# Kernel tuning notes

Measured on AMD Instinct MI355X. Metric: run time of the kernel, lower is better.

Reference implementation:

```python
import jax, jax.numpy as jnp
import numpy as np

H = 256
B, S = 8, 2048
WIN = 16


def setup_inputs() -> dict:
    key = jax.random.key(0)
    k1, k2, k3, k4, k5 = jax.random.split(key, 5)
    bound = 1.0 / np.sqrt(H)  # torch nn.RNN init range
    x = jax.random.normal(k1, (B, S, H), dtype=jnp.float32)
    W_ih = jax.random.uniform(k2, (H, H), jnp.float32, -bound, bound)
    W_hh = jax.random.uniform(k3, (H, H), jnp.float32, -bound, bound)
    b_ih = jax.random.uniform(k4, (H,), jnp.float32, -bound, bound)
    b_hh = jax.random.uniform(k5, (H,), jnp.float32, -bound, bound)
    return {"x": x, "W_ih": W_ih, "W_hh": W_hh, "b_ih": b_ih, "b_hh": b_hh, "window": WIN}


def reference(x, W_ih, W_hh, b_ih, b_hh, window):
    # Original: get_K builds [B, S, window, H] overlapping windows (left-padded
    # with window-1 zeros), runs an RNN over each length-`window` sequence with
    # h0 = 0, and keeps the last hidden state -> [B, S, H].
    # Equivalent streaming form: at step k of the window, every position t
    # consumes xpad[:, t + k]; so slice a shifted view of the padded input and
    # update all B*S hidden states at once (never materializing the windows).
    b, s, h = x.shape
    xpad = jnp.pad(x, ((0, 0), (window - 1, 0), (0, 0)))  # [B, S+W-1, H]

    def step(hid, k):
        xk = jax.lax.dynamic_slice(xpad, (0, k, 0), (b, s, h))  # [B, S, H]
        hid = jnp.tanh(xk @ W_ih.T + b_ih + hid @ W_hh.T + b_hh)
        return hid, None

    h0 = jnp.zeros((b, s, h), dtype=x.dtype)
    h_last, _ = jax.lax.scan(step, h0, jnp.arange(window))
    return h_last  # [B, S, H]
```

## Files before the change

### kernel.cpp

```cpp
#include <hip/hip_runtime.h>

#define HDIM 256
#define SEQ 2048
#define TPOS 32

typedef _Float16 half8_t __attribute__((ext_vector_type(8)));
typedef float floatx16 __attribute__((ext_vector_type(16)));

#define U_PITCH 1024
#define H_PITCH 512
#define U_ROWS 47
#define H0_OFF (U_ROWS * U_PITCH)
#define H1_OFF (H0_OFF + 32 * H_PITCH)
#define LDS_BYTES (H0_OFF + 2 * 32 * H_PITCH)

static __device__ __forceinline__ float exp2f_fast(float x) {
  float r; asm("v_exp_f32 %0, %1" : "=v"(r) : "v"(x)); return r;
}
static __device__ __forceinline__ float rcpf_fast(float x) {
  float r; asm("v_rcp_f32 %0, %1" : "=v"(r) : "v"(x)); return r;
}
static __device__ __forceinline__ float tanhf_fast(float x) {
  float e = exp2f_fast(x * 2.8853900817779268f);
  return 1.0f - 2.0f * rcpf_fast(e + 1.0f);
}
static __device__ __forceinline__ unsigned pkh(float a, float b) {
  return __builtin_bit_cast(unsigned, __builtin_amdgcn_cvt_pkrtz(a, b));
}

__global__ __launch_bounds__(256, 2) void winrnn_kernel(
    const float* __restrict__ x, const float* __restrict__ W_ih,
    const float* __restrict__ W_hh, const float* __restrict__ b_ih,
    const float* __restrict__ b_hh, float* __restrict__ out) {
  extern __shared__ char smem[];
  const int tid = threadIdx.x;
  const int w = tid >> 6;
  const int lane = tid & 63;
  const int l31 = lane & 31;
  const int hi = lane >> 5;

  const int wg = blockIdx.x;
  const int batch = wg >> 6;
  const int t0 = (wg & 63) * TPOS;
  const float* xb = x + (size_t)batch * SEQ * HDIM;

  const int jbase = w * 64;
  const int p_loc = l31;
  const int hswz = l31 << 4;

  {
    char* xl = smem + H0_OFF;
#pragma unroll
    for (int it = 0; it < 16; ++it) {
      int idx = tid + it * 256;
      int row = idx >> 6;
      int c4 = idx & 63;
      int xi = t0 - 15 + row;
      float4 v = make_float4(0.f, 0.f, 0.f, 0.f);
      if (row < U_ROWS && xi >= 0)
        v = *reinterpret_cast<const float4*>(xb + (size_t)xi * HDIM + c4 * 4);
      uint2 u;
      u.x = pkh(v.x, v.y);
      u.y = pkh(v.z, v.w);
      *reinterpret_cast<uint2*>(xl + row * H_PITCH + ((c4 * 8) ^ ((row & 31) << 4))) = u;
    }
  }

  half8_t Wf[2][16];
#pragma unroll
  for (int jt = 0; jt < 2; ++jt)
#pragma unroll
    for (int kt = 0; kt < 16; ++kt) {
      const float* wp = W_ih + (size_t)(jbase + jt * 32 + l31) * HDIM + kt * 16 + hi * 8;
      float4 a = *reinterpret_cast<const float4*>(wp);
      float4 b = *reinterpret_cast<const float4*>(wp + 4);
      uint4 uu;
      uu.x = pkh(a.x, a.y); uu.y = pkh(a.z, a.w);
      uu.z = pkh(b.x, b.y); uu.w = pkh(b.z, b.w);
      Wf[jt][kt] = __builtin_bit_cast(half8_t, uu);
    }

  float4 biasf[2][4];
#pragma unroll
  for (int jt = 0; jt < 2; ++jt)
#pragma unroll
    for (int g = 0; g < 4; ++g) {
      int j0 = jbase + jt * 32 + g * 8 + hi * 4;
      float4 bi = *reinterpret_cast<const float4*>(b_ih + j0);
      float4 bh = *reinterpret_cast<const float4*>(b_hh + j0);
      biasf[jt][g] = make_float4(bi.x + bh.x, bi.y + bh.y, bi.z + bh.z, bi.w + bh.w);
    }

  __syncthreads();

  {
    const char* xl = smem + H0_OFF;
    char* Ul = smem;
#pragma unroll
    for (int s = 0; s < 2; ++s) {
      int prow = s * 32 + l31;
      floatx16 acc0, acc1;
#pragma unroll
      for (int g = 0; g < 4; ++g) {
        acc0[4*g+0] = biasf[0][g].x; acc0[4*g+1] = biasf[0][g].y;
        acc0[4*g+2] = biasf[0][g].z; acc0[4*g+3] = biasf[0][g].w;
        acc1[4*g+0] = biasf[1][g].x; acc1[4*g+1] = biasf[1][g].y;
        acc1[4*g+2] = biasf[1][g].z; acc1[4*g+3] = biasf[1][g].w;
      }
#pragma unroll
      for (int kt = 0; kt < 16; ++kt) {
        half8_t xB = *reinterpret_cast<const half8_t*>(
            xl + prow * H_PITCH + ((kt * 32 + hi * 16) ^ ((prow & 31) << 4)));
        acc0 = __builtin_amdgcn_mfma_f32_32x32x16_f16(Wf[0][kt], xB, acc0, 0, 0, 0);
        acc1 = __builtin_amdgcn_mfma_f32_32x32x16_f16(Wf[1][kt], xB, acc1, 0, 0, 0);
      }
      if (prow < U_ROWS) {
#pragma unroll
        for (int jt = 0; jt < 2; ++jt)
#pragma unroll
          for (int g = 0; g < 4; ++g) {
            int j0 = jbase + jt * 32 + g * 8 + hi * 4;
            float4 st;
            const floatx16& ac = jt ? acc1 : acc0;
            st.x = ac[4*g+0]; st.y = ac[4*g+1]; st.z = ac[4*g+2]; st.w = ac[4*g+3];
            *reinterpret_cast<float4*>(Ul + prow * U_PITCH + ((j0 * 4) ^ ((prow & 31) << 4))) = st;
          }
      }
    }
  }

#pragma unroll
  for (int jt = 0; jt < 2; ++jt)
#pragma unroll
    for (int kt = 0; kt < 16; ++kt) {
      const float* wp = W_hh + (size_t)(jbase + jt * 32 + l31) * HDIM + kt * 16 + hi * 8;
      float4 a = *reinterpret_cast<const float4*>(wp);
      float4 b = *reinterpret_cast<const float4*>(wp + 4);
      uint4 uu;
      uu.x = pkh(a.x, a.y); uu.y = pkh(a.z, a.w);
      uu.z = pkh(b.x, b.y); uu.w = pkh(b.z, b.w);
      Wf[jt][kt] = __builtin_bit_cast(half8_t, uu);
    }

  __syncthreads();

  const char* Ul = smem;
  char* hb0 = smem + H0_OFF;
  char* hb1 = smem + H1_OFF;

  floatx16 acc0, acc1;
  for (int k = 0; k < 16; ++k) {
    int urow = p_loc + k;
    int uswz = (urow & 31) << 4;
#pragma unroll
    for (int g = 0; g < 4; ++g) {
      int j00 = (jbase + g * 8 + hi * 4) * 4;
      float4 u0 = *reinterpret_cast<const float4*>(Ul + urow * U_PITCH + (j00 ^ uswz));
      float4 u1 = *reinterpret_cast<const float4*>(Ul + urow * U_PITCH + ((j00 + 128) ^ uswz));
      acc0[4*g+0] = u0.x; acc0[4*g+1] = u0.y; acc0[4*g+2] = u0.z; acc0[4*g+3] = u0.w;
      acc1[4*g+0] = u1.x; acc1[4*g+1] = u1.y; acc1[4*g+2] = u1.z; acc1[4*g+3] = u1.w;
    }
    if (k > 0) {
      const char* hr = ((k & 1) ? hb0 : hb1);
#pragma unroll
      for (int kt = 0; kt < 16; ++kt) {
        half8_t hB = *reinterpret_cast<const half8_t*>(
            hr + p_loc * H_PITCH + ((kt * 32 + hi * 16) ^ hswz));
        acc0 = __builtin_amdgcn_mfma_f32_32x32x16_f16(Wf[0][kt], hB, acc0, 0, 0, 0);
        acc1 = __builtin_amdgcn_mfma_f32_32x32x16_f16(Wf[1][kt], hB, acc1, 0, 0, 0);
      }
    }
    if (k < 15) {
      char* hw = ((k & 1) ? hb1 : hb0);
#pragma unroll
      for (int jt = 0; jt < 2; ++jt) {
        const floatx16& ac = jt ? acc1 : acc0;
#pragma unroll
        for (int g = 0; g < 4; ++g) {
          float ta = tanhf_fast(ac[4*g+0]);
          float tb = tanhf_fast(ac[4*g+1]);
          float tc = tanhf_fast(ac[4*g+2]);
          float td = tanhf_fast(ac[4*g+3]);
          uint2 u; u.x = pkh(ta, tb); u.y = pkh(tc, td);
          int jb = (jbase + jt * 32 + g * 8 + hi * 4) * 2;
          *reinterpret_cast<uint2*>(hw + p_loc * H_PITCH + (jb ^ hswz)) = u;
        }
      }
      __syncthreads();
    }
  }

  __syncthreads();
  {
    char* ol = smem + H0_OFF;
    const int oswz = (p_loc & 31) << 4;
#pragma unroll
    for (int jt = 0; jt < 2; ++jt) {
      const floatx16& ac = jt ? acc1 : acc0;
#pragma unroll
      for (int g = 0; g < 4; ++g) {
        float4 st;
        st.x = tanhf_fast(ac[4*g+0]); st.y = tanhf_fast(ac[4*g+1]);
        st.z = tanhf_fast(ac[4*g+2]); st.w = tanhf_fast(ac[4*g+3]);
        int jb = (jbase + jt * 32 + g * 8 + hi * 4) * 4;
        *reinterpret_cast<float4*>(ol + p_loc * 1024 + (jb ^ oswz)) = st;
      }
    }
  }
  __syncthreads();
  {
    const char* ol = smem + H0_OFF;
    float* ob = out + ((size_t)batch * SEQ + t0) * HDIM;
#pragma unroll
    for (int it = 0; it < 8; ++it) {
      int idx = tid + it * 256;
      int row = idx >> 6;
      int c = idx & 63;
      float4 v = *reinterpret_cast<const float4*>(
          ol + row * 1024 + ((c * 16) ^ ((row & 31) << 4)));
      *reinterpret_cast<float4*>(ob + (size_t)row * HDIM + c * 4) = v;
    }
  }
}

extern "C" void kernel_launch(void* const* d_in, const int* in_sizes, int n_in,
                              void* d_out, int out_size, void* d_ws, size_t ws_size,
                              hipStream_t stream) {
  const float* x    = (const float*)d_in[0];
  const float* W_ih = (const float*)d_in[1];
  const float* W_hh = (const float*)d_in[2];
  const float* b_ih = (const float*)d_in[3];
  const float* b_hh = (const float*)d_in[4];
  float* out = (float*)d_out;
  static_assert(2 * LDS_BYTES <= 160 * 1024, "need 2 WGs/CU");
  hipFuncSetAttribute(reinterpret_cast<const void*>(winrnn_kernel),
                      hipFuncAttributeMaxDynamicSharedMemorySize, LDS_BYTES);
  winrnn_kernel<<<dim3(512), dim3(256), LDS_BYTES, stream>>>(x, W_ih, W_hh, b_ih, b_hh, out);
}
```

Baseline: 73.37 us.

## Store input projections in fp16, split MFMA chains, use rational tanh

Input-projection results U are now stored in LDS as fp16 rather than fp32, which halves U_PITCH, shrinks LDS use and cuts LDS traffic. The recurrent MFMA loop is split into two independent accumulator chains that are summed at the end, shortening the dependent-MFMA latency chain. tanh is replaced with a clamped Padé rational approximation that needs one reciprocal and no exp. The x-staging loop also drops iterations that only wrote rows past U_ROWS. The cost is lower precision for the pre-activations and an approximate tanh whose error near the clamp is larger.

```diff
diff --git a/kernel.cpp b/kernel.cpp
--- a/kernel.cpp
+++ b/kernel.cpp
@@ -5,24 +5,25 @@
 #define TPOS 32
 
 typedef _Float16 half8_t __attribute__((ext_vector_type(8)));
+typedef _Float16 half4_t __attribute__((ext_vector_type(4)));
 typedef float floatx16 __attribute__((ext_vector_type(16)));
 
-#define U_PITCH 1024
+#define U_PITCH 512
 #define H_PITCH 512
 #define U_ROWS 47
 #define H0_OFF (U_ROWS * U_PITCH)
 #define H1_OFF (H0_OFF + 32 * H_PITCH)
 #define LDS_BYTES (H0_OFF + 2 * 32 * H_PITCH)
 
-static __device__ __forceinline__ float exp2f_fast(float x) {
-  float r; asm("v_exp_f32 %0, %1" : "=v"(r) : "v"(x)); return r;
-}
 static __device__ __forceinline__ float rcpf_fast(float x) {
   float r; asm("v_rcp_f32 %0, %1" : "=v"(r) : "v"(x)); return r;
 }
 static __device__ __forceinline__ float tanhf_fast(float x) {
-  float e = exp2f_fast(x * 2.8853900817779268f);
-  return 1.0f - 2.0f * rcpf_fast(e + 1.0f);
+  x = fminf(fmaxf(x, -4.97f), 4.97f);
+  float t = x * x;
+  float N = ((t + 378.f) * t + 17325.f) * t + 135135.f;
+  float D = ((28.f * t + 3150.f) * t + 62370.f) * t + 135135.f;
+  return (x * N) * rcpf_fast(D);
 }
 static __device__ __forceinline__ unsigned pkh(float a, float b) {
   return __builtin_bit_cast(unsigned, __builtin_amdgcn_cvt_pkrtz(a, b));
@@ -51,18 +52,20 @@
   {
     char* xl = smem + H0_OFF;
 #pragma unroll
-    for (int it = 0; it < 16; ++it) {
+    for (int it = 0; it < 12; ++it) {
       int idx = tid + it * 256;
       int row = idx >> 6;
       int c4 = idx & 63;
       int xi = t0 - 15 + row;
-      float4 v = make_float4(0.f, 0.f, 0.f, 0.f);
-      if (row < U_ROWS && xi >= 0)
-        v = *reinterpret_cast<const float4*>(xb + (size_t)xi * HDIM + c4 * 4);
-      uint2 u;
-      u.x = pkh(v.x, v.y);
-      u.y = pkh(v.z, v.w);
-      *reinterpret_cast<uint2*>(xl + row * H_PITCH + ((c4 * 8) ^ ((row & 31) << 4))) = u;
+      if (row < U_ROWS) {
+        float4 v = make_float4(0.f, 0.f, 0.f, 0.f);
+        if (xi >= 0)
+          v = *reinterpret_cast<const float4*>(xb + (size_t)xi * HDIM + c4 * 4);
+        uint2 u;
+        u.x = pkh(v.x, v.y);
+        u.y = pkh(v.z, v.w);
+        *reinterpret_cast<uint2*>(xl + row * H_PITCH + ((c4 * 8) ^ ((row & 31) << 4))) = u;
+      }
     }
   }
 
@@ -115,15 +118,17 @@
         acc1 = __builtin_amdgcn_mfma_f32_32x32x16_f16(Wf[1][kt], xB, acc1, 0, 0, 0);
       }
       if (prow < U_ROWS) {
+        int uswz = (prow & 31) << 4;
 #pragma unroll
         for (int jt = 0; jt < 2; ++jt)
 #pragma unroll
           for (int g = 0; g < 4; ++g) {
+            const floatx16& ac = jt ? acc1 : acc0;
+            uint2 st;
+            st.x = pkh(ac[4*g+0], ac[4*g+1]);
+            st.y = pkh(ac[4*g+2], ac[4*g+3]);
             int j0 = jbase + jt * 32 + g * 8 + hi * 4;
-            float4 st;
-            const floatx16& ac = jt ? acc1 : acc0;
-            st.x = ac[4*g+0]; st.y = ac[4*g+1]; st.z = ac[4*g+2]; st.w = ac[4*g+3];
-            *reinterpret_cast<float4*>(Ul + prow * U_PITCH + ((j0 * 4) ^ ((prow & 31) << 4))) = st;
+            *reinterpret_cast<uint2*>(Ul + prow * U_PITCH + ((j0 * 2) ^ uswz)) = st;
           }
       }
     }
@@ -154,21 +159,32 @@
     int uswz = (urow & 31) << 4;
 #pragma unroll
     for (int g = 0; g < 4; ++g) {
-      int j00 = (jbase + g * 8 + hi * 4) * 4;
-      float4 u0 = *reinterpret_cast<const float4*>(Ul + urow * U_PITCH + (j00 ^ uswz));
-      float4 u1 = *reinterpret_cast<const float4*>(Ul + urow * U_PITCH + ((j00 + 128) ^ uswz));
-      acc0[4*g+0] = u0.x; acc0[4*g+1] = u0.y; acc0[4*g+2] = u0.z; acc0[4*g+3] = u0.w;
-      acc1[4*g+0] = u1.x; acc1[4*g+1] = u1.y; acc1[4*g+2] = u1.z; acc1[4*g+3] = u1.w;
+      int j00 = (jbase + g * 8 + hi * 4) * 2;
+      half4_t u0 = __builtin_bit_cast(half4_t, *reinterpret_cast<const uint2*>(
+          Ul + urow * U_PITCH + (j00 ^ uswz)));
+      half4_t u1 = __builtin_bit_cast(half4_t, *reinterpret_cast<const uint2*>(
+          Ul + urow * U_PITCH + ((j00 + 64) ^ uswz)));
+      acc0[4*g+0] = (float)u0[0]; acc0[4*g+1] = (float)u0[1];
+      acc0[4*g+2] = (float)u0[2]; acc0[4*g+3] = (float)u0[3];
+      acc1[4*g+0] = (float)u1[0]; acc1[4*g+1] = (float)u1[1];
+      acc1[4*g+2] = (float)u1[2]; acc1[4*g+3] = (float)u1[3];
     }
     if (k > 0) {
       const char* hr = ((k & 1) ? hb0 : hb1);
-#pragma unroll
-      for (int kt = 0; kt < 16; ++kt) {
+      floatx16 acc0b = {}, acc1b = {};
+#pragma unroll
+      for (int kt = 0; kt < 8; ++kt) {
         half8_t hB = *reinterpret_cast<const half8_t*>(
             hr + p_loc * H_PITCH + ((kt * 32 + hi * 16) ^ hswz));
-        acc0 = __builtin_amdgcn_mfma_f32_32x32x16_f16(Wf[0][kt], hB, acc0, 0, 0, 0);
-        acc1 = __builtin_amdgcn_mfma_f32_32x32x16_f16(Wf[1][kt], hB, acc1, 0, 0, 0);
-      }
+        half8_t hB2 = *reinterpret_cast<const half8_t*>(
+            hr + p_loc * H_PITCH + (((kt + 8) * 32 + hi * 16) ^ hswz));
+        acc0  = __builtin_amdgcn_mfma_f32_32x32x16_f16(Wf[0][kt],     hB,  acc0,  0, 0, 0);
+        acc0b = __builtin_amdgcn_mfma_f32_32x32x16_f16(Wf[0][kt + 8], hB2, acc0b, 0, 0, 0);
+        acc1  = __builtin_amdgcn_mfma_f32_32x32x16_f16(Wf[1][kt],     hB,  acc1,  0, 0, 0);
+        acc1b = __builtin_amdgcn_mfma_f32_32x32x16_f16(Wf[1][kt + 8], hB2, acc1b, 0, 0, 0);
+      }
+      acc0 += acc0b;
+      acc1 += acc1b;
     }
     if (k < 15) {
       char* hw = ((k & 1) ? hb1 : hb0);
@@ -193,7 +209,7 @@
   __syncthreads();
   {
     char* ol = smem + H0_OFF;
-    const int oswz = (p_loc & 31) << 4;
+    const int oswz = p_loc << 4;
 #pragma unroll
     for (int jt = 0; jt < 2; ++jt) {
       const floatx16& ac = jt ? acc1 : acc0;
@@ -202,8 +218,8 @@
         float4 st;
         st.x = tanhf_fast(ac[4*g+0]); st.y = tanhf_fast(ac[4*g+1]);
         st.z = tanhf_fast(ac[4*g+2]); st.w = tanhf_fast(ac[4*g+3]);
-        int jb = (jbase + jt * 32 + g * 8 + hi * 4) * 4;
-        *reinterpret_cast<float4*>(ol + p_loc * 1024 + (jb ^ oswz)) = st;
+        int jb4 = (jbase + jt * 32 + g * 8 + hi * 4) * 4;
+        *reinterpret_cast<float4*>(ol + p_loc * 1024 + (jb4 ^ oswz)) = st;
       }
     }
   }
@@ -232,7 +248,7 @@
   const float* b_ih = (const float*)d_in[3];
   const float* b_hh = (const float*)d_in[4];
   float* out = (float*)d_out;
-  static_assert(2 * LDS_BYTES <= 160 * 1024, "need 2 WGs/CU");
+  static_assert(2 * LDS_BYTES <= 160 * 1024, "need 2 WGs/CU with slack");
   hipFuncSetAttribute(reinterpret_cast<const void*>(winrnn_kernel),
                       hipFuncAttributeMaxDynamicSharedMemorySize, LDS_BYTES);
   winrnn_kernel<<<dim3(512), dim3(256), LDS_BYTES, stream>>>(x, W_ih, W_hh, b_ih, b_hh, out);
```

Measured after the change: 81.80 us. +11.5%, slower.
